# Optimization experiments

Hardware: AMD Instinct MI355X
Metric: run time of the kernel (lower is better)

Reference implementation:

```python
import jax, jax.numpy as jnp
import numpy as np

N = 50000
E = 800000
IN_FEAT = 256
HIDDEN = 256
NUM_CLASS = 10
NUM_GRAPHS = 512
LAYERS = 2


def setup_inputs() -> dict:
    key = jax.random.key(0)
    ks = jax.random.split(key, 10)
    x = jax.random.normal(ks[0], (N, IN_FEAT), dtype=jnp.float32)
    edge_index = jax.random.randint(ks[1], (2, E), 0, N, dtype=jnp.int32)
    batch = jnp.sort(jax.random.randint(ks[2], (N,), 0, NUM_GRAPHS, dtype=jnp.int32))
    s_in = 1.0 / np.sqrt(IN_FEAT)
    s_h = 1.0 / np.sqrt(HIDDEN)
    enc_W = jax.random.uniform(ks[3], (IN_FEAT, HIDDEN), jnp.float32, -s_in, s_in)
    enc_b = jax.random.uniform(ks[4], (HIDDEN,), jnp.float32, -s_in, s_in)
    conv_W = jax.random.uniform(ks[5], (LAYERS, HIDDEN, HIDDEN), jnp.float32, -s_h, s_h)
    conv_b = jax.random.uniform(ks[6], (LAYERS, HIDDEN), jnp.float32, -s_h, s_h)
    out_W = jax.random.uniform(ks[7], (HIDDEN, NUM_CLASS), jnp.float32, -s_h, s_h)
    out_b = jax.random.uniform(ks[8], (NUM_CLASS,), jnp.float32, -s_h, s_h)
    return {"x": x, "edge_index": edge_index, "batch": batch,
            "enc_W": enc_W, "enc_b": enc_b,
            "conv_W": conv_W, "conv_b": conv_b,
            "out_W": out_W, "out_b": out_b}


def _gcn_conv(x, row, col, deg_norm_edge, W, b):
    # PyG GCNConv: linear transform, then normalized scatter-add aggregation.
    h = x @ W                                   # [N, H]
    msg = h[row] * deg_norm_edge[:, None]       # [E+N, H] gather + scale
    out = jax.ops.segment_sum(msg, col, num_segments=N)  # scatter-add
    return out + b


def reference(x, edge_index, batch, enc_W, enc_b, conv_W, conv_b, out_W, out_b):
    # self-loops appended once (same structure every layer)
    loops = jnp.arange(N, dtype=edge_index.dtype)
    row = jnp.concatenate([edge_index[0], loops])  # source
    col = jnp.concatenate([edge_index[1], loops])  # target
    deg = jax.ops.segment_sum(jnp.ones_like(col, dtype=x.dtype), col, num_segments=N)
    dinv = jnp.where(deg > 0, jax.lax.rsqrt(deg), 0.0)
    norm = dinv[row] * dinv[col]                # symmetric GCN normalization per edge

    h = x @ enc_W + enc_b
    for i in range(LAYERS):
        h = jax.nn.relu(_gcn_conv(h, row, col, norm, conv_W[i], conv_b[i]))

    # global_mean_pool over `batch` segment ids
    sums = jax.ops.segment_sum(h, batch, num_segments=NUM_GRAPHS)
    cnts = jax.ops.segment_sum(jnp.ones((N,), dtype=h.dtype), batch, num_segments=NUM_GRAPHS)
    pooled = sums / jnp.maximum(cnts, 1.0)[:, None]

    # dropout is identity in eval mode
    return pooled @ out_W + out_b
```

## Files before the change

kernel.cpp:

```cpp
#include <hip/hip_runtime.h>

#define NN 50000
#define NE 800000
#define HD 256
#define NG 512
#define NC 10
#define TILES ((NN + 31) / 32)
#define NP 196
#define HB 200
#define CHUNK (NE / HB)
#define NODES_PER_HB (NN / HB)

typedef unsigned short u16;
typedef unsigned char u8;
typedef short v8s __attribute__((ext_vector_type(8)));
typedef float v4f __attribute__((ext_vector_type(4)));
typedef float v2f __attribute__((ext_vector_type(2)));
typedef u16 v4u __attribute__((ext_vector_type(4)));
typedef u16 v8u __attribute__((ext_vector_type(8)));

static __device__ __forceinline__ float bf2f(u16 u) {
    return __uint_as_float(((unsigned)u) << 16);
}
static __device__ __forceinline__ u16 f2bf(float f) {
    unsigned u = __float_as_uint(f);
    unsigned r = (u + 0x7fffu + ((u >> 16) & 1u)) >> 16;
    return (u16)r;
}
static __device__ __forceinline__ int clampi(int v, int lo, int hi) {
    return min(max(v, lo), hi);
}
static __device__ __forceinline__ float ldf(const void* p, size_t i, int isbf) {
    return isbf ? bf2f(((const u16*)p)[i]) : ((const float*)p)[i];
}

static __device__ __forceinline__ u8 f32_to_fp8(float f) {
#if __has_builtin(__builtin_amdgcn_cvt_pk_fp8_f32)
    int r = __builtin_amdgcn_cvt_pk_fp8_f32(f, f, 0, false);
    return (u8)(r & 0xff);
#else
    float a = fabsf(f);
    unsigned s = (__float_as_uint(f) >> 31) << 7;
    if (a < 0.0009765625f) return (u8)s;
    a = fminf(a, 448.f);
    if (a < 0.015625f) {
        int m = (int)(a * 512.f + 0.5f);
        return (u8)(s | min(m, 7));
    }
    unsigned u = __float_as_uint(a);
    unsigned r = u + 0x0007FFFFu + ((u >> 20) & 1u);
    int e = (int)(r >> 23) - 127 + 7;
    if (e > 15) return (u8)(s | 0x7E);
    unsigned m = (r >> 20) & 7u;
    return (u8)(s | ((unsigned)e << 3) | m);
#endif
}
static __device__ __forceinline__ v4f fp8x4_to_f32(unsigned v) {
#if __has_builtin(__builtin_amdgcn_cvt_pk_f32_fp8)
    v2f lo = __builtin_amdgcn_cvt_pk_f32_fp8(v, false);
    v2f hi = __builtin_amdgcn_cvt_pk_f32_fp8(v, true);
    return (v4f){lo[0], lo[1], hi[0], hi[1]};
#else
    v4f o;
#pragma unroll
    for (int j = 0; j < 4; j++) {
        unsigned b = (v >> (8 * j)) & 0xffu;
        unsigned e = (b >> 3) & 15u, m = b & 7u;
        float val = e ? __uint_as_float(((e + 120u) << 23) | (m << 20))
                      : (float)m * 0.001953125f;
        o[j] = (b & 0x80u) ? -val : val;
    }
    return o;
#endif
}

static __device__ __forceinline__ void gload_lds16(const void* g, void* l) {
#if __has_builtin(__builtin_amdgcn_global_load_lds)
    __builtin_amdgcn_global_load_lds(
        (const __attribute__((address_space(1))) void*)g,
        (__attribute__((address_space(3))) void*)l, 16, 0, 0);
#else
    *(v8s*)(l) = *(const v8s*)(g);
#endif
}

static __device__ __forceinline__ int detect_mode_block(
        const u16* __restrict__ xu, int* sh) {
    if (threadIdx.x == 0) sh[0] = 0;
    __syncthreads();
    int bad = 0;
    for (int i = threadIdx.x; i < 4096; i += 256) {
        float v = bf2f(xu[2 * i]);
        float av = fabsf(v);
        if (av > 100.f || (av < 1e-3f && av != 0.f)) bad++;
    }
    atomicAdd(sh, bad);
    __syncthreads();
    return (sh[0] > 1024) ? 0 : 1;
}

__global__ void k_prep(const u16* __restrict__ xu,
                       const void* __restrict__ enc_W, const void* __restrict__ conv_W,
                       const void* __restrict__ enc_b, const void* __restrict__ conv_b,
                       const void* __restrict__ out_b,
                       u16* __restrict__ Wp, float* __restrict__ biasf,
                       int* __restrict__ modep) {
    __shared__ int sh[1];
    int md = detect_mode_block(xu, sh);
    int b = blockIdx.x;
    if (b < 768) {
        int wi = b >> 8;
        int n = b & 255, k = threadIdx.x;
        const void* W = (wi == 0) ? enc_W : conv_W;
        size_t off = (wi == 0) ? 0 : (size_t)(wi - 1) * HD * HD;
        int nt = n >> 4, m = n & 15;
        int ks = k >> 5, q = (k >> 3) & 3, j = k & 7;
        size_t idx = ((((size_t)nt * 8 + ks) * 64) + q * 16 + m) * 8 + j;
        Wp[(size_t)wi * HD * HD + idx] = f2bf(ldf(W, off + (size_t)k * HD + n, md));
    } else {
        for (int j = threadIdx.x; j < 768 + NC; j += 256) {
            float v = (j < 256) ? ldf(enc_b, j, md)
                    : (j < 768) ? ldf(conv_b, j - 256, md)
                                : ldf(out_b, j - 768, md);
            biasf[j] = v;
        }
        if (threadIdx.x == 0) modep[0] = md;
    }
}

static __device__ __forceinline__ void hist_body(
        int b, const int* __restrict__ ecol, const int* __restrict__ batch,
        int* __restrict__ bh, int* __restrict__ gptr, int* hist) {
    int tid = threadIdx.x;
    if (tid < NP) hist[tid] = 0;
    __syncthreads();
    int e0 = b * CHUNK;
    for (int i = tid; i < CHUNK; i += 256) {
        int c = clampi(ecol[e0 + i], 0, NN - 1);
        atomicAdd(&hist[c >> 8], 1);
    }
    int n0 = b * NODES_PER_HB;
    for (int i = tid; i < NODES_PER_HB; i += 256) {
        int idx = n0 + i;
        int bb = clampi(batch[idx], 0, NG - 1);
        int bp = (idx == 0) ? -1 : clampi(batch[idx - 1], 0, NG - 1);
        for (int g = bp + 1; g <= bb; g++) gptr[g] = idx;
        if (idx == NN - 1)
            for (int g = bb + 1; g <= NG; g++) gptr[g] = NN;
    }
    __syncthreads();
    if (tid < NP) bh[(size_t)tid * HB + b] = hist[tid];
}

static __device__ __forceinline__ void scat_body(
        int b, const int* __restrict__ erow, const int* __restrict__ ecol,
        const int* __restrict__ pptr, const int* __restrict__ base,
        unsigned* __restrict__ pairbuf, int* lfill) {
    int tid = threadIdx.x;
    if (tid < NP) lfill[tid] = 0;
    __syncthreads();
    int e0 = b * CHUNK;
    for (int i = tid; i < CHUNK; i += 256) {
        int c = clampi(ecol[e0 + i], 0, NN - 1);
        int rw = clampi(erow[e0 + i], 0, NN - 1);
        int p = c >> 8;
        int r = atomicAdd(&lfill[p], 1);
        int pos = pptr[p] + base[(size_t)p * HB + b] + r;
        pairbuf[pos] = ((unsigned)rw << 8) | (unsigned)(c & 255);
    }
}

static __device__ __forceinline__ void gemm_body(
        int bid, u16* As, const void* __restrict__ A, const u16* __restrict__ Wp,
        const float* __restrict__ biasf, void* __restrict__ out,
        int M, int hasBias, int outFp8, int amode) {
    int tid = threadIdx.x;
    int wave = tid >> 6;
    int lane = tid & 63;
    int row0 = bid * 32;
    if (row0 >= M) return;
    int m = lane & 15, q = lane >> 4;

    if (amode) {
#if __has_builtin(__builtin_amdgcn_global_load_lds)
#pragma unroll
        for (int j = 0; j < 4; j++) {
            int slot = j * 256 + tid;
            int row = slot >> 5, sb = slot & 31;
            int gb = sb ^ (row & 7);
            const u16* src = (const u16*)A +
                (size_t)min(row0 + row, M - 1) * HD + gb * 8;
            u16* dst = As + ((size_t)j * 256 + wave * 64) * 8;
            gload_lds16(src, dst);
        }
#else
#pragma unroll
        for (int j = 0; j < 4; j++) {
            int slot = j * 256 + tid;
            int row = slot >> 5, sb = slot & 31;
            int gb = sb ^ (row & 7);
            const u16* src = (const u16*)A +
                (size_t)min(row0 + row, M - 1) * HD + gb * 8;
            *(v8s*)&As[(size_t)slot * 8] = *(const v8s*)src;
        }
#endif
    } else {
#pragma unroll
        for (int j = 0; j < 4; j++) {
            int slot = j * 256 + tid;
            int row = slot >> 5, sb = slot & 31;
            int gb = sb ^ (row & 7);
            const float* af = (const float*)A +
                (size_t)min(row0 + row, M - 1) * HD + gb * 8;
            v4f x0 = *(const v4f*)af;
            v4f x1 = *(const v4f*)(af + 4);
            v8s v;
            v[0] = (short)f2bf(x0[0]); v[1] = (short)f2bf(x0[1]);
            v[2] = (short)f2bf(x0[2]); v[3] = (short)f2bf(x0[3]);
            v[4] = (short)f2bf(x1[0]); v[5] = (short)f2bf(x1[1]);
            v[6] = (short)f2bf(x1[2]); v[7] = (short)f2bf(x1[3]);
            *(v8s*)&As[(size_t)slot * 8] = v;
        }
    }
    __syncthreads();

    v4f acc[2][4];
#pragma unroll
    for (int i = 0; i < 2; i++)
#pragma unroll
        for (int j = 0; j < 4; j++) acc[i][j] = (v4f){0.f, 0.f, 0.f, 0.f};

    const u16* wp = Wp + (size_t)wave * 4 * 8 * 64 * 8;

#pragma unroll
    for (int ks = 0; ks < 8; ks++) {
        v8s bfr[4];
#pragma unroll
        for (int nt = 0; nt < 4; nt++)
            bfr[nt] = *(const v8s*)(wp + ((size_t)(nt * 8 + ks) * 64 + lane) * 8);
        v8s a[2];
#pragma unroll
        for (int mt = 0; mt < 2; mt++) {
            int row = mt * 16 + m;
            a[mt] = *(const v8s*)&As[(size_t)row * 256 +
                                     (size_t)(((ks * 4 + q) ^ (m & 7)) * 8)];
        }
#pragma unroll
        for (int mt = 0; mt < 2; mt++)
#pragma unroll
            for (int nt = 0; nt < 4; nt++)
                acc[mt][nt] = __builtin_amdgcn_mfma_f32_16x16x32_bf16(
                    a[mt], bfr[nt], acc[mt][nt], 0, 0, 0);
    }
    if (outFp8) {
#pragma unroll
        for (int mt = 0; mt < 2; mt++) {
#pragma unroll
            for (int nt = 0; nt < 4; nt++) {
                int ocol = wave * 64 + nt * 16 + m;
#pragma unroll
                for (int r = 0; r < 4; r++) {
                    int orow = row0 + mt * 16 + q * 4 + r;
                    if (orow < M)
                        ((u8*)out)[(size_t)orow * HD + ocol] =
                            f32_to_fp8(acc[mt][nt][r] * 32.f);
                }
            }
        }
    } else {
#pragma unroll
        for (int mt = 0; mt < 2; mt++) {
#pragma unroll
            for (int nt = 0; nt < 4; nt++) {
                int ocol = wave * 64 + nt * 16 + m;
                float badd = hasBias ? biasf[ocol] : 0.f;
#pragma unroll
                for (int r = 0; r < 4; r++) {
                    int orow = row0 + mt * 16 + q * 4 + r;
                    if (orow < M)
                        ((u16*)out)[(size_t)orow * HD + ocol] =
                            f2bf(acc[mt][nt][r] + badd);
                }
            }
        }
    }
}

__global__ __launch_bounds__(256) void k_gemm(
        const void* __restrict__ A, const u16* __restrict__ Wp,
        const float* __restrict__ biasf, void* __restrict__ out,
        int M, int hasBias, int outFp8,
        const int* __restrict__ modep, int forceBf) {
    __shared__ u16 As[32 * 256];
    gemm_body(blockIdx.x, As, A, Wp, biasf, out, M, hasBias, outFp8,
              forceBf ? 1 : modep[0]);
}

__global__ __launch_bounds__(256) void k_hist(
        const int* __restrict__ ecol, const int* __restrict__ batch,
        int* __restrict__ bh, int* __restrict__ gptr) {
    __shared__ int hist[NP];
    hist_body(blockIdx.x, ecol, batch, bh, gptr, hist);
}

__global__ __launch_bounds__(256) void k_scat(
        const int* __restrict__ erow, const int* __restrict__ ecol,
        const int* __restrict__ pptr, const int* __restrict__ base,
        unsigned* __restrict__ pairbuf) {
    __shared__ int lfill[NP];
    scat_body(blockIdx.x, erow, ecol, pptr, base, pairbuf, lfill);
}

__global__ __launch_bounds__(256) void k_gemm_hist(
        const void* __restrict__ A, const u16* __restrict__ Wp,
        const float* __restrict__ biasf, void* __restrict__ out,
        int M, int hasBias, const int* __restrict__ modep, int forceBf,
        const int* __restrict__ ecol, const int* __restrict__ batch,
        int* __restrict__ bh, int* __restrict__ gptr) {
    __shared__ u16 As[32 * 256];
    __shared__ int hist[NP];
    if (blockIdx.x < HB) {
        hist_body(blockIdx.x, ecol, batch, bh, gptr, hist);
    } else {
        gemm_body(blockIdx.x - HB, As, A, Wp, biasf, out, M, hasBias, 0,
                  forceBf ? 1 : modep[0]);
    }
}

__global__ __launch_bounds__(256) void k_scat_gemm1(
        const void* __restrict__ A, const u16* __restrict__ Wp,
        void* __restrict__ out, int M,
        const int* __restrict__ erow, const int* __restrict__ ecol,
        const int* __restrict__ pptr, const int* __restrict__ base,
        unsigned* __restrict__ pairbuf) {
    __shared__ u16 As[32 * 256];
    __shared__ int lfill[NP];
    if (blockIdx.x < HB) {
        scat_body(blockIdx.x, erow, ecol, pptr, base, pairbuf, lfill);
    } else {
        gemm_body(blockIdx.x - HB, As, A, Wp, nullptr, out, M, 0, 1, 1);
    }
}

static __device__ __forceinline__ void agg_node(
        const u8* __restrict__ t, const int* __restrict__ cptr,
        const int* __restrict__ csrc, const float* __restrict__ dinv,
        const float* __restrict__ biasf, int node, int lane, float* o) {
    int half = lane >> 5;
    int f0 = (lane & 31) * 8;
    const u8* tf = t + f0;
    float dn = dinv[node];
    float a[8];
#pragma unroll
    for (int k = 0; k < 8; k++) a[k] = 0.f;

    if (half == 0) {
        uint2 sv = *(const uint2*)(tf + (size_t)node * HD);
        v4f lo = fp8x4_to_f32(sv.x), hi = fp8x4_to_f32(sv.y);
#pragma unroll
        for (int k = 0; k < 4; k++) {
            a[k] += lo[k] * dn;
            a[k + 4] += hi[k] * dn;
        }
    }

    int e0 = cptr[node], e1 = cptr[node + 1];
    e1 = clampi(e1, 0, NE);
    e0 = clampi(e0, 0, e1);
    int e = e0;
    for (; e + 16 <= e1; e += 16) {
        int s[8];
#pragma unroll
        for (int j = 0; j < 8; j++)
            s[j] = clampi(csrc[e + 2 * j + half], 0, NN - 1);
        uint2 rv[8];
        float wv[8];
#pragma unroll
        for (int j = 0; j < 8; j++) {
            rv[j] = *(const uint2*)(tf + (size_t)s[j] * HD);
            wv[j] = dinv[s[j]];
        }
#pragma unroll
        for (int j = 0; j < 8; j++) {
            v4f lo = fp8x4_to_f32(rv[j].x), hi = fp8x4_to_f32(rv[j].y);
#pragma unroll
            for (int k = 0; k < 4; k++) {
                a[k] = fmaf(lo[k], wv[j], a[k]);
                a[k + 4] = fmaf(hi[k], wv[j], a[k + 4]);
            }
        }
    }
    for (; e + 2 <= e1; e += 2) {
        int s = clampi(csrc[e + half], 0, NN - 1);
        uint2 rv = *(const uint2*)(tf + (size_t)s * HD);
        float wv = dinv[s];
        v4f lo = fp8x4_to_f32(rv.x), hi = fp8x4_to_f32(rv.y);
#pragma unroll
        for (int k = 0; k < 4; k++) {
            a[k] = fmaf(lo[k], wv, a[k]);
            a[k + 4] = fmaf(hi[k], wv, a[k + 4]);
        }
    }
    if (e < e1 && half == 0) {
        int s = clampi(csrc[e], 0, NN - 1);
        uint2 rv = *(const uint2*)(tf + (size_t)s * HD);
        float wv = dinv[s];
        v4f lo = fp8x4_to_f32(rv.x), hi = fp8x4_to_f32(rv.y);
#pragma unroll
        for (int k = 0; k < 4; k++) {
            a[k] = fmaf(lo[k], wv, a[k]);
            a[k + 4] = fmaf(hi[k], wv, a[k + 4]);
        }
    }
#pragma unroll
    for (int k = 0; k < 8; k++) a[k] += __shfl_xor(a[k], 32, 64);

    float sc = dn * 0.03125f;
    v4f b0 = *(const v4f*)(biasf + f0);
    v4f b1 = *(const v4f*)(biasf + f0 + 4);
#pragma unroll
    for (int k = 0; k < 4; k++) {
        o[k] = fmaxf(fmaf(a[k], sc, b0[k]), 0.f);
        o[k + 4] = fmaxf(fmaf(a[k + 4], sc, b1[k]), 0.f);
    }
}

__global__ __launch_bounds__(256) void k_aggregate2(
        const u8* __restrict__ t, const int* __restrict__ cptr,
        const int* __restrict__ csrc, const float* __restrict__ dinv,
        const float* __restrict__ biasf, u16* __restrict__ out) {
    int wave = threadIdx.x >> 6, lane = threadIdx.x & 63;
    int node = blockIdx.x * 4 + wave;
    if (node >= NN) return;
    float o[8];
    agg_node(t, cptr, csrc, dinv, biasf, node, lane, o);
    if (lane < 32) {
        v8u pk;
#pragma unroll
        for (int k = 0; k < 8; k++) pk[k] = f2bf(o[k]);
        *(v8u*)(out + (size_t)node * HD + lane * 8) = pk;
    }
}

__global__ __launch_bounds__(256) void k_scanA(
        const int* __restrict__ bh, int* __restrict__ base, int* __restrict__ ptot) {
    int p = blockIdx.x, t = threadIdx.x;
    int v = (t < HB) ? bh[(size_t)p * HB + t] : 0;
    __shared__ int sh[256];
    sh[t] = v;
    __syncthreads();
    for (int off = 1; off < 256; off <<= 1) {
        int x = (t >= off) ? sh[t - off] : 0;
        __syncthreads();
        sh[t] += x;
        __syncthreads();
    }
    if (t < HB) base[(size_t)p * HB + t] = sh[t] - v;
    if (t == 0) ptot[p] = sh[255];
}

__global__ __launch_bounds__(256) void k_scanB(
        const int* __restrict__ ptot, int* __restrict__ pptr) {
    int t = threadIdx.x;
    int v = (t < NP) ? ptot[t] : 0;
    __shared__ int sh[256];
    sh[t] = v;
    __syncthreads();
    for (int off = 1; off < 256; off <<= 1) {
        int x = (t >= off) ? sh[t - off] : 0;
        __syncthreads();
        sh[t] += x;
        __syncthreads();
    }
    if (t < NP) pptr[t] = sh[t] - v;
    if (t == 0) pptr[NP] = sh[255];
}

__global__ __launch_bounds__(256) void k_part2(
        const int* __restrict__ pptr, const unsigned* __restrict__ pairbuf,
        int* __restrict__ cptr, float* __restrict__ dinv, int* __restrict__ csrc) {
    int p = blockIdx.x, t = threadIdx.x;
    int seg0 = pptr[p], seg1 = pptr[p + 1];
    __shared__ int hist[256], sums[256], fill[256];
    hist[t] = 0;
    fill[t] = 0;
    __syncthreads();
    for (int i = seg0 + t; i < seg1; i += 256)
        atomicAdd(&hist[pairbuf[i] & 255], 1);
    __syncthreads();
    int d = hist[t];
    sums[t] = d;
    __syncthreads();
    for (int off = 1; off < 256; off <<= 1) {
        int x = (t >= off) ? sums[t - off] : 0;
        __syncthreads();
        sums[t] += x;
        __syncthreads();
    }
    int ex = sums[t] - d;
    int c = p * 256 + t;
    if (c < NN) {
        cptr[c] = seg0 + ex;
        dinv[c] = rsqrtf((float)(d + 1));
    }
    if (p == NP - 1 && t == 0) cptr[NN] = NE;
    __syncthreads();
    sums[t] = ex;
    __syncthreads();
    for (int i = seg0 + t; i < seg1; i += 256) {
        unsigned v = pairbuf[i];
        int cl = v & 255;
        int r = atomicAdd(&fill[cl], 1);
        csrc[seg0 + sums[cl] + r] = (int)(v >> 8);
    }
}

__global__ __launch_bounds__(256) void k_head(
        const u16* __restrict__ h, const int* __restrict__ gptr,
        const void* __restrict__ W, const float* __restrict__ biasf,
        void* __restrict__ outv, const int* __restrict__ modep) {
    int md = modep[0];
    int g = blockIdx.x, f = threadIdx.x;
    int hi = clampi(gptr[g + 1], 0, NN);
    int lo = clampi(gptr[g], 0, hi);
    float s0 = 0.f, s1 = 0.f, s2 = 0.f, s3 = 0.f;
    int i = lo;
    for (; i + 4 <= hi; i += 4) {
        s0 += bf2f(h[(size_t)i * HD + f]);
        s1 += bf2f(h[(size_t)(i + 1) * HD + f]);
        s2 += bf2f(h[(size_t)(i + 2) * HD + f]);
        s3 += bf2f(h[(size_t)(i + 3) * HD + f]);
    }
    for (; i < hi; i++) s0 += bf2f(h[(size_t)i * HD + f]);
    __shared__ float ps[256];
    ps[f] = ((s0 + s1) + (s2 + s3)) / fmaxf((float)(hi - lo), 1.0f);
    __syncthreads();
    if (threadIdx.x < 64) {
        int lane = threadIdx.x;
        float acc[NC];
#pragma unroll
        for (int c = 0; c < NC; c++) acc[c] = 0.f;
        for (int k = lane; k < HD; k += 64) {
            float p = ps[k];
#pragma unroll
            for (int c = 0; c < NC; c++) acc[c] += p * ldf(W, (size_t)k * NC + c, md);
        }
#pragma unroll
        for (int c = 0; c < NC; c++) {
            for (int off = 32; off > 0; off >>= 1)
                acc[c] += __shfl_down(acc[c], off, 64);
        }
        if (lane == 0) {
#pragma unroll
            for (int c = 0; c < NC; c++) {
                float vv = acc[c] + biasf[768 + c];
                if (md) ((u16*)outv)[g * NC + c] = f2bf(vv);
                else    ((float*)outv)[g * NC + c] = vv;
            }
        }
    }
}

extern "C" void kernel_launch(void* const* d_in, const int* in_sizes, int n_in,
                              void* d_out, int out_size, void* d_ws, size_t ws_size,
                              hipStream_t stream) {
    const void* x      = d_in[0];
    const int*  ei     = (const int*)d_in[1];
    const int*  batch  = (const int*)d_in[2];
    const void* enc_W  = d_in[3];
    const void* enc_b  = d_in[4];
    const void* conv_W = d_in[5];
    const void* conv_b = d_in[6];
    const void* out_W  = d_in[7];
    const void* out_b  = d_in[8];

    char* w = (char*)d_ws;
    auto alloc = [&](size_t b) { char* p = w; w += (b + 255) & ~(size_t)255; return p; };
    int*   mode   = (int*)alloc(256);
    float* dinv   = (float*)alloc(NN * 4);
    int*   cptr   = (int*)alloc((NN + 1) * 4);
    int*   gptr   = (int*)alloc((NG + 1) * 4);
    int*   csrc   = (int*)alloc((size_t)NE * 4);
    u16*   Wp     = (u16*)alloc((size_t)3 * HD * HD * 2);
    float* biasf  = (float*)alloc(778 * 4);
    u16*   hbuf   = (u16*)alloc((size_t)NN * HD * 2);
    size_t scratch_need = ((size_t)2 * NP * HB + 2 * NP + 1) * 4 + (size_t)NE * 4 + 1024;
    size_t used = (size_t)(w - (char*)d_ws);
    bool fused = (used + scratch_need <= ws_size);
    char* sb = fused ? alloc(scratch_need) : (char*)hbuf;
    int* bh   = (int*)sb;
    int* base = bh + (size_t)NP * HB;
    int* ptot = base + (size_t)NP * HB;
    int* pptr = ptot + NP;
    unsigned* pairbuf = (unsigned*)(pptr + NP + 1);
    u8* tbuf = (u8*)d_in[0];

    const int* erow = ei;
    const int* ecol = ei + NE;

    k_prep<<<769, 256, 0, stream>>>((const u16*)x, enc_W, conv_W, enc_b,
                                    conv_b, out_b, Wp, biasf, mode);

    if (fused) {
        k_gemm_hist<<<HB + TILES, 256, 0, stream>>>(
            x, Wp, biasf, hbuf, NN, 1, mode, 0, ecol, batch, bh, gptr);
        k_scanA<<<NP, 256, 0, stream>>>(bh, base, ptot);
        k_scanB<<<1, 256, 0, stream>>>(ptot, pptr);
        k_scat_gemm1<<<HB + TILES, 256, 0, stream>>>(
            hbuf, Wp + (size_t)HD * HD, tbuf, NN, erow, ecol, pptr, base, pairbuf);
        k_part2<<<NP, 256, 0, stream>>>(pptr, pairbuf, cptr, dinv, csrc);
    } else {
        k_hist<<<HB, 256, 0, stream>>>(ecol, batch, bh, gptr);
        k_scanA<<<NP, 256, 0, stream>>>(bh, base, ptot);
        k_scanB<<<1, 256, 0, stream>>>(ptot, pptr);
        k_scat<<<HB, 256, 0, stream>>>(erow, ecol, pptr, base, pairbuf);
        k_part2<<<NP, 256, 0, stream>>>(pptr, pairbuf, cptr, dinv, csrc);
        k_gemm<<<TILES, 256, 0, stream>>>(x, Wp, biasf, hbuf, NN, 1, 0, mode, 0);
        k_gemm<<<TILES, 256, 0, stream>>>(hbuf, Wp + (size_t)HD * HD, nullptr,
                                          tbuf, NN, 0, 1, mode, 1);
    }
    k_aggregate2<<<(NN + 3) / 4, 256, 0, stream>>>(tbuf, cptr, csrc, dinv,
                                                   biasf + 256, hbuf);
    k_gemm<<<TILES, 256, 0, stream>>>(hbuf, Wp + (size_t)2 * HD * HD, nullptr,
                                      tbuf, NN, 0, 1, mode, 1);
    k_aggregate2<<<(NN + 3) / 4, 256, 0, stream>>>(tbuf, cptr, csrc, dinv,
                                                   biasf + 256 + HD, hbuf);
    k_head<<<NG, 256, 0, stream>>>(hbuf, gptr, out_W, biasf, d_out, mode);
}
```

Before: 283.6 us.

## Fold histogram prefix scans into scatter and partition kernels

Removes the two separate scan kernels and has every scatter block and partition block recompute the per-partition offsets directly from the block histogram. This eliminates two kernel launches and the intermediate base/pptr buffers in the CSR build. In exchange, each block redundantly rereads the whole histogram with strided per-thread accesses and runs a shared-memory scan, which adds work to the scatter phase. A bounds guard on the pair buffer write is also added.

```diff
diff --git a/kernel.cpp b/kernel.cpp
--- a/kernel.cpp
+++ b/kernel.cpp
@@ -154,10 +154,29 @@
 
 static __device__ __forceinline__ void scat_body(
         int b, const int* __restrict__ erow, const int* __restrict__ ecol,
-        const int* __restrict__ pptr, const int* __restrict__ base,
-        unsigned* __restrict__ pairbuf, int* lfill) {
+        const int* __restrict__ bh, unsigned* __restrict__ pairbuf,
+        int* sums, int* lbase, int* lfill) {
     int tid = threadIdx.x;
     if (tid < NP) lfill[tid] = 0;
+    int tot = 0, pre = 0;
+    if (tid < NP) {
+        const int* rowp = bh + (size_t)tid * HB;
+#pragma unroll 8
+        for (int i = 0; i < HB; i++) {
+            int v = rowp[i];
+            if (i < b) pre += v;
+            tot += v;
+        }
+    }
+    sums[tid] = tot;
+    __syncthreads();
+    for (int off = 1; off < 256; off <<= 1) {
+        int x = (tid >= off) ? sums[tid - off] : 0;
+        __syncthreads();
+        sums[tid] += x;
+        __syncthreads();
+    }
+    if (tid < NP) lbase[tid] = (sums[tid] - tot) + pre;
     __syncthreads();
     int e0 = b * CHUNK;
     for (int i = tid; i < CHUNK; i += 256) {
@@ -165,8 +184,9 @@
         int rw = clampi(erow[e0 + i], 0, NN - 1);
         int p = c >> 8;
         int r = atomicAdd(&lfill[p], 1);
-        int pos = pptr[p] + base[(size_t)p * HB + b] + r;
-        pairbuf[pos] = ((unsigned)rw << 8) | (unsigned)(c & 255);
+        int pos = lbase[p] + r;
+        if (pos >= 0 && pos < NE)
+            pairbuf[pos] = ((unsigned)rw << 8) | (unsigned)(c & 255);
     }
 }
 
@@ -305,10 +325,9 @@
 
 __global__ __launch_bounds__(256) void k_scat(
         const int* __restrict__ erow, const int* __restrict__ ecol,
-        const int* __restrict__ pptr, const int* __restrict__ base,
-        unsigned* __restrict__ pairbuf) {
-    __shared__ int lfill[NP];
-    scat_body(blockIdx.x, erow, ecol, pptr, base, pairbuf, lfill);
+        const int* __restrict__ bh, unsigned* __restrict__ pairbuf) {
+    __shared__ int sums[256], lbase[256], lfill[256];
+    scat_body(blockIdx.x, erow, ecol, bh, pairbuf, sums, lbase, lfill);
 }
 
 __global__ __launch_bounds__(256) void k_gemm_hist(
@@ -331,12 +350,11 @@
         const void* __restrict__ A, const u16* __restrict__ Wp,
         void* __restrict__ out, int M,
         const int* __restrict__ erow, const int* __restrict__ ecol,
-        const int* __restrict__ pptr, const int* __restrict__ base,
-        unsigned* __restrict__ pairbuf) {
+        const int* __restrict__ bh, unsigned* __restrict__ pairbuf) {
     __shared__ u16 As[32 * 256];
-    __shared__ int lfill[NP];
+    __shared__ int sums[256], lbase[256], lfill[256];
     if (blockIdx.x < HB) {
-        scat_body(blockIdx.x, erow, ecol, pptr, base, pairbuf, lfill);
+        scat_body(blockIdx.x, erow, ecol, bh, pairbuf, sums, lbase, lfill);
     } else {
         gemm_body(blockIdx.x - HB, As, A, Wp, nullptr, out, M, 0, 1, 1);
     }
@@ -442,48 +460,29 @@
     }
 }
 
-__global__ __launch_bounds__(256) void k_scanA(
-        const int* __restrict__ bh, int* __restrict__ base, int* __restrict__ ptot) {
-    int p = blockIdx.x, t = threadIdx.x;
-    int v = (t < HB) ? bh[(size_t)p * HB + t] : 0;
-    __shared__ int sh[256];
-    sh[t] = v;
-    __syncthreads();
-    for (int off = 1; off < 256; off <<= 1) {
-        int x = (t >= off) ? sh[t - off] : 0;
-        __syncthreads();
-        sh[t] += x;
-        __syncthreads();
-    }
-    if (t < HB) base[(size_t)p * HB + t] = sh[t] - v;
-    if (t == 0) ptot[p] = sh[255];
-}
-
-__global__ __launch_bounds__(256) void k_scanB(
-        const int* __restrict__ ptot, int* __restrict__ pptr) {
-    int t = threadIdx.x;
-    int v = (t < NP) ? ptot[t] : 0;
-    __shared__ int sh[256];
-    sh[t] = v;
-    __syncthreads();
-    for (int off = 1; off < 256; off <<= 1) {
-        int x = (t >= off) ? sh[t - off] : 0;
-        __syncthreads();
-        sh[t] += x;
-        __syncthreads();
-    }
-    if (t < NP) pptr[t] = sh[t] - v;
-    if (t == 0) pptr[NP] = sh[255];
-}
-
 __global__ __launch_bounds__(256) void k_part2(
-        const int* __restrict__ pptr, const unsigned* __restrict__ pairbuf,
+        const int* __restrict__ bh, const unsigned* __restrict__ pairbuf,
         int* __restrict__ cptr, float* __restrict__ dinv, int* __restrict__ csrc) {
     int p = blockIdx.x, t = threadIdx.x;
-    int seg0 = pptr[p], seg1 = pptr[p + 1];
-    __shared__ int hist[256], sums[256], fill[256];
+    __shared__ int sums[256], hist[256], fill[256];
     hist[t] = 0;
     fill[t] = 0;
+    int tot = 0;
+    if (t < NP) {
+        const int* rowp = bh + (size_t)t * HB;
+#pragma unroll 8
+        for (int i = 0; i < HB; i++) tot += rowp[i];
+    }
+    sums[t] = tot;
+    __syncthreads();
+    for (int off = 1; off < 256; off <<= 1) {
+        int x = (t >= off) ? sums[t - off] : 0;
+        __syncthreads();
+        sums[t] += x;
+        __syncthreads();
+    }
+    int seg0 = (p > 0) ? sums[p - 1] : 0;
+    int seg1 = sums[p];
     __syncthreads();
     for (int i = seg0 + t; i < seg1; i += 256)
         atomicAdd(&hist[pairbuf[i] & 255], 1);
@@ -584,15 +583,12 @@
     u16*   Wp     = (u16*)alloc((size_t)3 * HD * HD * 2);
     float* biasf  = (float*)alloc(778 * 4);
     u16*   hbuf   = (u16*)alloc((size_t)NN * HD * 2);
-    size_t scratch_need = ((size_t)2 * NP * HB + 2 * NP + 1) * 4 + (size_t)NE * 4 + 1024;
+    size_t scratch_need = (size_t)NP * HB * 4 + (size_t)NE * 4 + 1024;
     size_t used = (size_t)(w - (char*)d_ws);
     bool fused = (used + scratch_need <= ws_size);
     char* sb = fused ? alloc(scratch_need) : (char*)hbuf;
     int* bh   = (int*)sb;
-    int* base = bh + (size_t)NP * HB;
-    int* ptot = base + (size_t)NP * HB;
-    int* pptr = ptot + NP;
-    unsigned* pairbuf = (unsigned*)(pptr + NP + 1);
+    unsigned* pairbuf = (unsigned*)(bh + (size_t)NP * HB);
     u8* tbuf = (u8*)d_in[0];
 
     const int* erow = ei;
@@ -604,17 +600,13 @@
     if (fused) {
         k_gemm_hist<<<HB + TILES, 256, 0, stream>>>(
             x, Wp, biasf, hbuf, NN, 1, mode, 0, ecol, batch, bh, gptr);
-        k_scanA<<<NP, 256, 0, stream>>>(bh, base, ptot);
-        k_scanB<<<1, 256, 0, stream>>>(ptot, pptr);
         k_scat_gemm1<<<HB + TILES, 256, 0, stream>>>(
-            hbuf, Wp + (size_t)HD * HD, tbuf, NN, erow, ecol, pptr, base, pairbuf);
-        k_part2<<<NP, 256, 0, stream>>>(pptr, pairbuf, cptr, dinv, csrc);
+            hbuf, Wp + (size_t)HD * HD, tbuf, NN, erow, ecol, bh, pairbuf);
+        k_part2<<<NP, 256, 0, stream>>>(bh, pairbuf, cptr, dinv, csrc);
     } else {
         k_hist<<<HB, 256, 0, stream>>>(ecol, batch, bh, gptr);
-        k_scanA<<<NP, 256, 0, stream>>>(bh, base, ptot);
-        k_scanB<<<1, 256, 0, stream>>>(ptot, pptr);
-        k_scat<<<HB, 256, 0, stream>>>(erow, ecol, pptr, base, pairbuf);
-        k_part2<<<NP, 256, 0, stream>>>(pptr, pairbuf, cptr, dinv, csrc);
+        k_scat<<<HB, 256, 0, stream>>>(erow, ecol, bh, pairbuf);
+        k_part2<<<NP, 256, 0, stream>>>(bh, pairbuf, cptr, dinv, csrc);
         k_gemm<<<TILES, 256, 0, stream>>>(x, Wp, biasf, hbuf, NN, 1, 0, mode, 0);
         k_gemm<<<TILES, 256, 0, stream>>>(hbuf, Wp + (size_t)HD * HD, nullptr,
                                           tbuf, NN, 0, 1, mode, 1);
```

After: 291.0 us. 2.6% more time.
